# Kernel optimization log

Hardware: AMD Instinct MI355X
Metric: run time of the kernel (lower is better)

Reference implementation:

```python
import jax, jax.numpy as jnp
import numpy as np
from jax import lax

IMG = 512            # image H = W
FH = FW = 32         # feature map spatial size
A = 9                # anchors per location (3 sizes x 3 ratios)
N = FH * FW * A      # total anchors = 9216
IOU_THR = 0.7
MIN_SCORE = 0.5
MIN_SIZE = 1e-3


def make_anchors():
    """Anchors in centroid format (cx, cy, w, h), ordered (H, W, A)."""
    stride = IMG / FH
    sizes = np.array([32.0, 64.0, 128.0])
    ratios = np.array([0.5, 1.0, 2.0])
    ws = (sizes[:, None] / np.sqrt(ratios)[None, :]).reshape(-1)  # (A,)
    hs = (sizes[:, None] * np.sqrt(ratios)[None, :]).reshape(-1)  # (A,)
    cx = (np.arange(FW) + 0.5) * stride
    cy = (np.arange(FH) + 0.5) * stride
    CX = np.broadcast_to(cx[None, :, None], (FH, FW, A))
    CY = np.broadcast_to(cy[:, None, None], (FH, FW, A))
    Wg = np.broadcast_to(ws[None, None, :], (FH, FW, A))
    Hg = np.broadcast_to(hs[None, None, :], (FH, FW, A))
    anc = np.stack([CX, CY, Wg, Hg], axis=-1).reshape(-1, 4)
    return jnp.asarray(anc, dtype=jnp.float32)


def pairwise_iou(b):
    # b: (N,4) corners x1,y1,x2,y2
    x1, y1, x2, y2 = b[:, 0], b[:, 1], b[:, 2], b[:, 3]
    area = (x2 - x1) * (y2 - y1)
    ix1 = jnp.maximum(x1[:, None], x1[None, :])
    iy1 = jnp.maximum(y1[:, None], y1[None, :])
    ix2 = jnp.minimum(x2[:, None], x2[None, :])
    iy2 = jnp.minimum(y2[:, None], y2[None, :])
    inter = jnp.maximum(ix2 - ix1, 0.0) * jnp.maximum(iy2 - iy1, 0.0)
    union = area[:, None] + area[None, :] - inter
    return inter / jnp.maximum(union, 1e-9)


def nms_keep(boxes, scores, valid):
    """Greedy NMS. Returns bool keep mask of shape (N,). Index decisions only."""
    s = jnp.where(valid, scores, -jnp.inf)
    order = jnp.argsort(-s)
    b = boxes[order]
    v = valid[order]
    ious = pairwise_iou(b)  # (N, N)
    idx = jnp.arange(N)

    def body(i, supp):
        keep_i = (~supp[i]) & v[i]
        return supp | (keep_i & (ious[i] > IOU_THR) & (idx > i))

    supp = lax.fori_loop(0, N, body, jnp.zeros(N, dtype=bool))
    keep_sorted = (~supp) & v
    return jnp.zeros(N, dtype=bool).at[order].set(keep_sorted)


def setup_inputs() -> dict:
    key = jax.random.key(0)
    ks = jax.random.split(key, 4)
    return {
        "feature_map": jax.random.normal(ks[0], (1, 256, FH, FW), jnp.float32),
        "conv1_w": jax.random.normal(ks[1], (512, 256, 3, 3), jnp.float32) * 0.02,
        "conv1_b": jnp.zeros((512,), jnp.float32),
        "conv2_w": jax.random.normal(ks[2], (A, 512), jnp.float32) * 0.01,
        "conv2_b": jnp.zeros((A,), jnp.float32),
        "conv3_w": jax.random.normal(ks[3], (4 * A, 512), jnp.float32) * 0.01,
        "conv3_b": jnp.zeros((4 * A,), jnp.float32),
    }


def reference(feature_map, conv1_w, conv1_b, conv2_w, conv2_b, conv3_w, conv3_b):
    anchors = make_anchors()  # (N,4) cx,cy,w,h

    # --- conv backbone head ---
    h = lax.conv_general_dilated(
        feature_map, conv1_w, (1, 1), "SAME",
        dimension_numbers=("NCHW", "OIHW", "NCHW"))
    h = jax.nn.relu(h + conv1_b[None, :, None, None])  # (1,512,H,W)

    scores = jax.nn.sigmoid(
        jnp.einsum("bchw,ac->bahw", h, conv2_w) + conv2_b[None, :, None, None])
    scores = scores.transpose(0, 2, 3, 1).reshape(-1)  # (N,) ordered (H,W,A)

    off = jnp.einsum("bchw,oc->bohw", h, conv3_w) + conv3_b[None, :, None, None]
    off = off.reshape(1, A, 4, FH, FW).transpose(0, 3, 4, 1, 2).reshape(-1, 4)

    acx, acy, aw, ah = anchors[:, 0], anchors[:, 1], anchors[:, 2], anchors[:, 3]
    cx = acx + off[:, 0] * aw
    cy = acy + off[:, 1] * ah
    bw = aw * jnp.exp(off[:, 2])
    bh = ah * jnp.exp(off[:, 3])
    boxes = jnp.stack([cx - bw / 2, cy - bh / 2, cx + bw / 2, cy + bh / 2], axis=1)

    # --- clip to image ---
    lo = jnp.array([0.0, 0.0, 0.0, 0.0], jnp.float32)
    hi = jnp.array([IMG, IMG, IMG, IMG], jnp.float32)
    boxes = jnp.clip(boxes, lo, hi)

    # --- remove small boxes + score threshold (as a mask, jit-safe) ---
    valid = ((boxes[:, 2] - boxes[:, 0]) >= MIN_SIZE) \
          & ((boxes[:, 3] - boxes[:, 1]) >= MIN_SIZE) \
          & (scores >= MIN_SCORE)

    # --- NMS (selection is index-based; no gradient through the decision) ---
    keep = nms_keep(lax.stop_gradient(boxes), lax.stop_gradient(scores), valid)

    out = jnp.concatenate(
        [boxes * keep[:, None].astype(boxes.dtype),
         (scores * keep.astype(scores.dtype))[:, None]], axis=1)  # (N,5)
    return out
```

## Files before the change

### kernel.cpp

```cpp
#include <hip/hip_runtime.h>
#include <math.h>

#define FHW   32
#define NA    9
#define NBOX  9216
#define C1    256
#define C2    512
#define KTOT  2304
#define KS    8
#define KCH   (KTOT / KS)
#define CAP   64
#define ECAP  12288

struct AnchorWH { float w[NA]; float h[NA]; };

#define FP_OFF    0u
#define WT_OFF    1183744u
#define HP_OFF    5902336u
#define BOX_OFF   22679552u
#define SC_OFF    22827008u
#define VL_OFF    22863872u
#define DEG_OFF   22900736u
#define ADJ_OFF   22937600u
#define NV_OFF    24117248u

__global__ __launch_bounds__(256) void k_prep(const float* __restrict__ fin,
                                              float* __restrict__ Fp,
                                              unsigned int* __restrict__ deg,
                                              unsigned int* __restrict__ nv,
                                              const float* __restrict__ w1,
                                              float* __restrict__ Wt) {
    if (blockIdx.x < 1156) {
        int idx = blockIdx.x * 256 + threadIdx.x;
        if (idx < 256 * 34 * 34) {
            int c   = idx / 1156;
            int rem = idx - c * 1156;
            int yy  = rem / 34;
            int xx  = rem - yy * 34;
            float v = 0.f;
            if (yy >= 1 && yy <= 32 && xx >= 1 && xx <= 32)
                v = fin[c * 1024 + (yy - 1) * 32 + (xx - 1)];
            Fp[idx] = v;
        }
        if (idx < NBOX) deg[idx] = 0u;
        if (idx == 0)   *nv = 0u;
    } else {
        __shared__ float tile[32][33];
        int tb  = blockIdx.x - 1156;
        int k0  = (tb % 72) * 32;
        int oc0 = (tb / 72) * 32;
        int t   = threadIdx.x;
        int r0 = t >> 5, c = t & 31;
        #pragma unroll
        for (int i = 0; i < 4; ++i) {
            int r = r0 + 8 * i;
            tile[r][c] = w1[(oc0 + r) * KTOT + k0 + c];
        }
        __syncthreads();
        #pragma unroll
        for (int i = 0; i < 4; ++i) {
            int kk = r0 + 8 * i;
            Wt[(k0 + kk) * C2 + oc0 + c] = tile[c][kk];
        }
    }
}

__global__ __launch_bounds__(256, 2) void k_gemm(const float* __restrict__ Fp,
                                                 const float* __restrict__ Wt,
                                                 float* __restrict__ hp) {
    const int id = blockIdx.x;
    const int bx = id >> 5, g = id & 31;
    const int by = g >> 3, kz = g & 7;
    const int p0  = bx * 64;
    const int oc0 = by * 128;
    const int k0b = kz * KCH;
    const int t  = threadIdx.x;
    const int ty = t >> 4, tx = t & 15;

    __shared__ float As[16][64];
    __shared__ float Bs[16][128];

    float acc[4][8];
    #pragma unroll
    for (int r = 0; r < 4; ++r)
        #pragma unroll
        for (int c = 0; c < 8; ++c) acc[r][c] = 0.f;

    for (int kt = 0; kt < KCH; kt += 16) {
        #pragma unroll
        for (int i = 0; i < 4; ++i) {
            int e  = t + 256 * i;
            int kk = e >> 6, pp = e & 63;
            int k   = k0b + kt + kk;
            int c   = k / 9;
            int kap = k - c * 9;
            int dy  = kap / 3;
            int dx  = kap - dy * 3;
            int p  = p0 + pp;
            int y  = p >> 5, x = p & 31;
            As[kk][pp] = Fp[(c * 34 + y + dy) * 34 + x + dx];
        }
        #pragma unroll
        for (int i = 0; i < 2; ++i) {
            int e4 = t + 256 * i;
            int kk = e4 >> 5, c4 = e4 & 31;
            *(float4*)&Bs[kk][c4 * 4] =
                *(const float4*)&Wt[(k0b + kt + kk) * C2 + oc0 + c4 * 4];
        }
        __syncthreads();
        #pragma unroll
        for (int kk = 0; kk < 16; ++kk) {
            float a[4], b[8];
            *(float4*)&a[0] = *(const float4*)&As[kk][ty * 4];
            *(float4*)&b[0] = *(const float4*)&Bs[kk][tx * 4];
            *(float4*)&b[4] = *(const float4*)&Bs[kk][tx * 4 + 64];
            #pragma unroll
            for (int r = 0; r < 4; ++r)
                #pragma unroll
                for (int c = 0; c < 8; ++c) acc[r][c] += a[r] * b[c];
        }
        __syncthreads();
    }
    #pragma unroll
    for (int r = 0; r < 4; ++r) {
        int p = p0 + ty * 4 + r;
        float* dst = hp + ((kz * 1024 + p) * C2 + oc0 + tx * 4);
        *(float4*)dst        = *(float4*)&acc[r][0];
        *(float4*)(dst + 64) = *(float4*)&acc[r][4];
    }
}

__global__ __launch_bounds__(256) void k_heads(const float* __restrict__ hp,
                                               const float* __restrict__ b1,
                                               const float* __restrict__ w2,
                                               const float* __restrict__ b2,
                                               const float* __restrict__ w3,
                                               const float* __restrict__ b3,
                                               float* __restrict__ boxes,
                                               float* __restrict__ scoresG,
                                               unsigned int* __restrict__ nv,
                                               unsigned int* __restrict__ vlist,
                                               AnchorWH awh) {
    const int p0 = blockIdx.x * 4;
    const int t  = threadIdx.x;
    __shared__ float hrow[4][C2];
    __shared__ float arr[4][45];

    #pragma unroll
    for (int px = 0; px < 4; ++px) {
        int p = p0 + px;
        #pragma unroll
        for (int i = 0; i < 2; ++i) {
            int c = t + 256 * i;
            float s = b1[c];
            #pragma unroll
            for (int ks = 0; ks < KS; ++ks) s += hp[(ks * 1024 + p) * C2 + c];
            hrow[px][c] = fmaxf(s, 0.f);
        }
    }
    __syncthreads();

    const int w = t >> 6, lane = t & 63;
    for (int job = w; job < 180; job += 4) {
        int px = job / 45, j = job - px * 45;
        const float* wp = (j < 9) ? (w2 + j * C2) : (w3 + (j - 9) * C2);
        float s = 0.f;
        #pragma unroll
        for (int i = 0; i < 8; ++i) s += hrow[px][lane + 64 * i] * wp[lane + 64 * i];
        #pragma unroll
        for (int d = 1; d < 64; d <<= 1) s += __shfl_xor(s, d, 64);
        if (lane == 0) arr[px][j] = s;
    }
    __syncthreads();

    if (t < 36) {
        int px = t / 9, a = t - px * 9;
        int p = p0 + px;
        float logit = arr[px][a] + b2[a];
        float score = 1.f / (1.f + expf(-logit));
        float o0 = arr[px][9 + a * 4 + 0] + b3[a * 4 + 0];
        float o1 = arr[px][9 + a * 4 + 1] + b3[a * 4 + 1];
        float o2 = arr[px][9 + a * 4 + 2] + b3[a * 4 + 2];
        float o3 = arr[px][9 + a * 4 + 3] + b3[a * 4 + 3];
        int y = p >> 5, x = p & 31;
        float ax = (x + 0.5f) * 16.f, ay = (y + 0.5f) * 16.f;
        float aw = awh.w[a], ah = awh.h[a];
        float cx = ax + o0 * aw;
        float cy = ay + o1 * ah;
        float bw = aw * expf(o2);
        float bh = ah * expf(o3);
        float x1 = fminf(fmaxf(cx - bw * 0.5f, 0.f), 512.f);
        float y1 = fminf(fmaxf(cy - bh * 0.5f, 0.f), 512.f);
        float x2 = fminf(fmaxf(cx + bw * 0.5f, 0.f), 512.f);
        float y2 = fminf(fmaxf(cy + bh * 0.5f, 0.f), 512.f);
        int n = p * 9 + a;
        float4 bx4; bx4.x = x1; bx4.y = y1; bx4.z = x2; bx4.w = y2;
        ((float4*)boxes)[n] = bx4;
        scoresG[n] = score;
        bool valid = (x2 - x1 >= 0.001f) && (y2 - y1 >= 0.001f) && (score >= 0.5f);
        if (valid) {
            unsigned int ci = atomicAdd(nv, 1u);
            vlist[ci] = (unsigned int)n;
        }
    }
}

__global__ __launch_bounds__(256) void k_adj(const unsigned int* __restrict__ nvp,
                                             const unsigned int* __restrict__ vlist,
                                             const float* __restrict__ boxes,
                                             const float* __restrict__ scoresG,
                                             unsigned int* __restrict__ deg,
                                             unsigned short* __restrict__ adj) {
    const int Nv = (int)*nvp;
    int b = blockIdx.x;
    int tv = (int)(sqrtf(2.f * b + 0.25f) - 0.5f);
    while ((tv + 1) * (tv + 2) / 2 <= b) tv++;
    while (tv * (tv + 1) / 2 > b) tv--;
    int tu = b - tv * (tv + 1) / 2;
    if (tv * 128 >= Nv) return;

    __shared__ float4 ub[128], vb[128];
    __shared__ float  us[128], vs[128];
    __shared__ int    uo[128], vo[128];
    int t = threadIdx.x;
    if (t < 128) {
        int gi = tu * 128 + t;
        if (gi < Nv) { int n = (int)vlist[gi]; ub[t] = ((const float4*)boxes)[n]; us[t] = scoresG[n]; uo[t] = n; }
        else us[t] = -1.f;
    } else {
        int tt = t - 128;
        int gj = tv * 128 + tt;
        if (gj < Nv) { int n = (int)vlist[gj]; vb[tt] = ((const float4*)boxes)[n]; vs[tt] = scoresG[n]; vo[tt] = n; }
        else vs[tt] = -1.f;
    }
    __syncthreads();

    for (int s = 0; s < 64; ++s) {
        int q  = t + 256 * s;
        int i  = q >> 7, jj = q & 127;
        if (tu == tv && i >= jj) continue;
        float su = us[i], sv = vs[jj];
        if (su < 0.f || sv < 0.f) continue;
        float4 bu = ub[i], bv = vb[jj];
        float au = (bu.z - bu.x) * (bu.w - bu.y);
        float av = (bv.z - bv.x) * (bv.w - bv.y);
        float ix1 = fmaxf(bu.x, bv.x), iy1 = fmaxf(bu.y, bv.y);
        float ix2 = fminf(bu.z, bv.z), iy2 = fminf(bu.w, bv.w);
        float inter = fmaxf(ix2 - ix1, 0.f) * fmaxf(iy2 - iy1, 0.f);
        float uni = au + av - inter;
        float iou = inter / fmaxf(uni, 1e-9f);
        if (iou > 0.7f) {
            int gi = tu * 128 + i, gj = tv * 128 + jj;
            bool uHigh = (su > sv) || (su == sv && uo[i] < vo[jj]);
            int lower = uHigh ? gj : gi;
            int upper = uHigh ? gi : gj;
            unsigned int slot = atomicAdd(&deg[lower], 1u);
            if (slot < CAP) adj[lower * CAP + slot] = (unsigned short)upper;
        }
    }
}

__global__ __launch_bounds__(512) void k_peel(const unsigned int* __restrict__ nvp,
                                              const unsigned int* __restrict__ vlist,
                                              const unsigned int* __restrict__ degG,
                                              const unsigned short* __restrict__ adjG,
                                              const float* __restrict__ boxes,
                                              const float* __restrict__ scoresG,
                                              float* __restrict__ out) {
    __shared__ unsigned char  st[NBOX];
    __shared__ unsigned char  degL[NBOX];
    __shared__ unsigned short offL[NBOX];
    __shared__ unsigned short csr[ECAP];
    __shared__ unsigned int   scratch[512];
    __shared__ int changed;
    const int t  = threadIdx.x;
    const int Nv = (int)*nvp;
    const int chunk = (Nv + 511) / 512;
    const int i0 = t * chunk;
    const int i1 = (i0 + chunk < Nv) ? (i0 + chunk) : Nv;

    unsigned int lsum = 0;
    for (int i = i0; i < i1; ++i) {
        unsigned int d = degG[i];
        if (d > CAP) d = CAP;
        degL[i] = (unsigned char)d;
        st[i] = 0;
        lsum += d;
    }
    scratch[t] = lsum;
    __syncthreads();
    for (int ofs = 1; ofs < 512; ofs <<= 1) {
        unsigned int v = (t >= ofs) ? scratch[t - ofs] : 0u;
        __syncthreads();
        scratch[t] += v;
        __syncthreads();
    }
    unsigned int base = scratch[t] - lsum;
    {
        unsigned int off = base;
        for (int i = i0; i < i1; ++i) {
            unsigned int o = (off < ECAP) ? off : ECAP;
            offL[i] = (unsigned short)o;
            int d = degL[i];
            int ld = (int)ECAP - (int)o; if (ld > d) ld = d; if (ld < 0) ld = 0;
            for (int s = 0; s < ld; ++s)
                csr[o + s] = adjG[i * CAP + s];
            off += d;
        }
    }
    __syncthreads();

    for (int round = 0; round < 256; ++round) {
        if (t == 0) changed = 0;
        __syncthreads();
        bool any = false;
        for (int i = i0; i < i1; ++i) {
            if (st[i] == 0) {
                int d   = degL[i];
                int off = offL[i];
                int ld  = (int)ECAP - off; if (ld > d) ld = d; if (ld < 0) ld = 0;
                bool kseen = false, useen = false;
                for (int s = 0; s < d; ++s) {
                    int j = (s < ld) ? (int)csr[off + s] : (int)adjG[i * CAP + s];
                    unsigned char v = st[j];
                    kseen |= (v == 1);
                    useen |= (v == 0);
                }
                if (kseen)       { st[i] = 2; any = true; }
                else if (!useen) { st[i] = 1; any = true; }
            }
        }
        if (any) changed = 1;
        __syncthreads();
        int c = changed;
        __syncthreads();
        if (!c) break;
    }

    for (int n = t; n < NBOX; n += 512) {
        out[n * 5 + 0] = 0.f; out[n * 5 + 1] = 0.f; out[n * 5 + 2] = 0.f;
        out[n * 5 + 3] = 0.f; out[n * 5 + 4] = 0.f;
    }
    __syncthreads();
    for (int i = t; i < Nv; i += 512) {
        if (st[i] == 1) {
            int n = (int)vlist[i];
            float4 b = ((const float4*)boxes)[n];
            out[n * 5 + 0] = b.x;
            out[n * 5 + 1] = b.y;
            out[n * 5 + 2] = b.z;
            out[n * 5 + 3] = b.w;
            out[n * 5 + 4] = scoresG[n];
        }
    }
}

extern "C" void kernel_launch(void* const* d_in, const int* in_sizes, int n_in,
                              void* d_out, int out_size, void* d_ws, size_t ws_size,
                              hipStream_t stream) {
    const float* fin = (const float*)d_in[0];
    const float* w1  = (const float*)d_in[1];
    const float* b1  = (const float*)d_in[2];
    const float* w2  = (const float*)d_in[3];
    const float* b2  = (const float*)d_in[4];
    const float* w3  = (const float*)d_in[5];
    const float* b3  = (const float*)d_in[6];
    float* out = (float*)d_out;

    char* ws = (char*)d_ws;
    float*          Fp    = (float*)(ws + FP_OFF);
    float*          Wt    = (float*)(ws + WT_OFF);
    float*          hp    = (float*)(ws + HP_OFF);
    float*          boxes = (float*)(ws + BOX_OFF);
    float*          sc    = (float*)(ws + SC_OFF);
    unsigned int*   vlist = (unsigned int*)(ws + VL_OFF);
    unsigned int*   deg   = (unsigned int*)(ws + DEG_OFF);
    unsigned short* adj   = (unsigned short*)(ws + ADJ_OFF);
    unsigned int*   nv    = (unsigned int*)(ws + NV_OFF);

    AnchorWH awh;
    {
        const double sizes[3]  = {32.0, 64.0, 128.0};
        const double ratios[3] = {0.5, 1.0, 2.0};
        for (int si = 0; si < 3; ++si)
            for (int ri = 0; ri < 3; ++ri) {
                awh.w[si * 3 + ri] = (float)(sizes[si] / sqrt(ratios[ri]));
                awh.h[si * 3 + ri] = (float)(sizes[si] * sqrt(ratios[ri]));
            }
    }

    k_prep<<<dim3(1156 + 72 * 16), 256, 0, stream>>>(fin, Fp, deg, nv, w1, Wt);
    k_gemm<<<dim3(512), 256, 0, stream>>>(Fp, Wt, hp);
    k_heads<<<dim3(256), 256, 0, stream>>>(hp, b1, w2, b2, w3, b3, boxes, sc, nv, vlist, awh);
    k_adj<<<dim3(72 * 73 / 2), 256, 0, stream>>>(nv, vlist, boxes, sc, deg, adj);
    k_peel<<<dim3(1), 512, 0, stream>>>(nv, vlist, deg, adj, boxes, sc, out);
}
```

Baseline: 229.3 us.

## Move output scatter out of single-block peel and trim peel round overhead

The single-block peel kernel no longer zeroes and writes the whole (N,5) output. It records keep flags in a global buffer, and a new grid-wide k_out kernel writes the masked boxes and scores in parallel. The peel loop now walks only still-undecided nodes through a per-thread bitmask and marks zero-degree nodes as kept up front. It also takes degree from CSR offset differences, enlarges the shared CSR capacity, and uses a per-round flag array so each round needs one barrier instead of three. The cost is one extra kernel launch, plus a round cap lowered from 256 to 96, which could end peeling early on very deep suppression chains.

```diff
diff --git a/kernel.cpp b/kernel.cpp
--- a/kernel.cpp
+++ b/kernel.cpp
@@ -10,7 +10,8 @@
 #define KS    8
 #define KCH   (KTOT / KS)
 #define CAP   64
-#define ECAP  12288
+#define ECAP  16384
+#define ROUNDS 96
 
 struct AnchorWH { float w[NA]; float h[NA]; };
 
@@ -22,11 +23,13 @@
 #define VL_OFF    22863872u
 #define DEG_OFF   22900736u
 #define ADJ_OFF   22937600u
-#define NV_OFF    24117248u
+#define KEEP_OFF  24117248u
+#define NV_OFF    24154112u
 
 __global__ __launch_bounds__(256) void k_prep(const float* __restrict__ fin,
                                               float* __restrict__ Fp,
                                               unsigned int* __restrict__ deg,
+                                              unsigned int* __restrict__ keepG,
                                               unsigned int* __restrict__ nv,
                                               const float* __restrict__ w1,
                                               float* __restrict__ Wt) {
@@ -42,7 +45,7 @@
                 v = fin[c * 1024 + (yy - 1) * 32 + (xx - 1)];
             Fp[idx] = v;
         }
-        if (idx < NBOX) deg[idx] = 0u;
+        if (idx < NBOX) { deg[idx] = 0u; keepG[idx] = 0u; }
         if (idx == 0)   *nv = 0u;
     } else {
         __shared__ float tile[32][33];
@@ -264,27 +267,25 @@
                                               const unsigned int* __restrict__ vlist,
                                               const unsigned int* __restrict__ degG,
                                               const unsigned short* __restrict__ adjG,
-                                              const float* __restrict__ boxes,
-                                              const float* __restrict__ scoresG,
-                                              float* __restrict__ out) {
+                                              unsigned int* __restrict__ keepG) {
+    __shared__ unsigned short offL[NBOX + 2];
     __shared__ unsigned char  st[NBOX];
-    __shared__ unsigned char  degL[NBOX];
-    __shared__ unsigned short offL[NBOX];
     __shared__ unsigned short csr[ECAP];
     __shared__ unsigned int   scratch[512];
-    __shared__ int changed;
+    __shared__ unsigned char  flags[ROUNDS];
     const int t  = threadIdx.x;
     const int Nv = (int)*nvp;
     const int chunk = (Nv + 511) / 512;
     const int i0 = t * chunk;
     const int i1 = (i0 + chunk < Nv) ? (i0 + chunk) : Nv;
 
+    if (t < ROUNDS) flags[t] = 0;
+
     unsigned int lsum = 0;
     for (int i = i0; i < i1; ++i) {
         unsigned int d = degG[i];
         if (d > CAP) d = CAP;
-        degL[i] = (unsigned char)d;
-        st[i] = 0;
+        st[i] = (unsigned char)d;
         lsum += d;
     }
     scratch[t] = lsum;
@@ -295,64 +296,72 @@
         scratch[t] += v;
         __syncthreads();
     }
-    unsigned int base = scratch[t] - lsum;
+    if (t == 511) {
+        unsigned int tot = scratch[511];
+        offL[Nv] = (unsigned short)(tot < ECAP ? tot : ECAP);
+    }
+    unsigned int amask = 0;
     {
-        unsigned int off = base;
+        unsigned int off = scratch[t] - lsum;
         for (int i = i0; i < i1; ++i) {
             unsigned int o = (off < ECAP) ? off : ECAP;
             offL[i] = (unsigned short)o;
-            int d = degL[i];
+            int d = st[i];
             int ld = (int)ECAP - (int)o; if (ld > d) ld = d; if (ld < 0) ld = 0;
             for (int s = 0; s < ld; ++s)
                 csr[o + s] = adjG[i * CAP + s];
             off += d;
+            if (d == 0) st[i] = 1;
+            else { st[i] = 0; amask |= 1u << (i - i0); }
         }
     }
     __syncthreads();
 
-    for (int round = 0; round < 256; ++round) {
-        if (t == 0) changed = 0;
-        __syncthreads();
+    for (int r = 0; r < ROUNDS; ++r) {
         bool any = false;
-        for (int i = i0; i < i1; ++i) {
-            if (st[i] == 0) {
-                int d   = degL[i];
-                int off = offL[i];
-                int ld  = (int)ECAP - off; if (ld > d) ld = d; if (ld < 0) ld = 0;
-                bool kseen = false, useen = false;
-                for (int s = 0; s < d; ++s) {
-                    int j = (s < ld) ? (int)csr[off + s] : (int)adjG[i * CAP + s];
-                    unsigned char v = st[j];
-                    kseen |= (v == 1);
-                    useen |= (v == 0);
-                }
-                if (kseen)       { st[i] = 2; any = true; }
-                else if (!useen) { st[i] = 1; any = true; }
+        unsigned int m = amask;
+        while (m) {
+            int b = __ffs(m) - 1; m &= m - 1;
+            int i = i0 + b;
+            int o = offL[i], on = offL[i + 1];
+            int d, ld;
+            if (on < ECAP) { d = on - o; ld = d; }
+            else {
+                unsigned int dg = degG[i]; d = (dg > CAP) ? CAP : (int)dg;
+                ld = (int)ECAP - o; if (ld < 0) ld = 0; if (ld > d) ld = d;
             }
-        }
-        if (any) changed = 1;
-        __syncthreads();
-        int c = changed;
-        __syncthreads();
-        if (!c) break;
-    }
-
-    for (int n = t; n < NBOX; n += 512) {
-        out[n * 5 + 0] = 0.f; out[n * 5 + 1] = 0.f; out[n * 5 + 2] = 0.f;
-        out[n * 5 + 3] = 0.f; out[n * 5 + 4] = 0.f;
-    }
-    __syncthreads();
-    for (int i = t; i < Nv; i += 512) {
-        if (st[i] == 1) {
-            int n = (int)vlist[i];
-            float4 b = ((const float4*)boxes)[n];
-            out[n * 5 + 0] = b.x;
-            out[n * 5 + 1] = b.y;
-            out[n * 5 + 2] = b.z;
-            out[n * 5 + 3] = b.w;
-            out[n * 5 + 4] = scoresG[n];
-        }
-    }
+            bool kseen = false, useen = false;
+            for (int s = 0; s < d; ++s) {
+                int j = (s < ld) ? (int)csr[o + s] : (int)adjG[i * CAP + s];
+                unsigned char v = st[j];
+                kseen |= (v == 1);
+                useen |= (v == 0);
+            }
+            if (kseen)       { st[i] = 2; any = true; amask &= ~(1u << b); }
+            else if (!useen) { st[i] = 1; any = true; amask &= ~(1u << b); }
+        }
+        if (any) flags[r] = 1;
+        __syncthreads();
+        if (!flags[r]) break;
+    }
+
+    for (int i = i0; i < i1; ++i)
+        if (st[i] == 1) keepG[vlist[i]] = 1u;
+}
+
+__global__ __launch_bounds__(256) void k_out(const float* __restrict__ boxes,
+                                             const float* __restrict__ scoresG,
+                                             const unsigned int* __restrict__ keepG,
+                                             float* __restrict__ out) {
+    int n = blockIdx.x * 256 + threadIdx.x;
+    if (n >= NBOX) return;
+    float k = keepG[n] ? 1.f : 0.f;
+    float4 b = ((const float4*)boxes)[n];
+    out[n * 5 + 0] = b.x * k;
+    out[n * 5 + 1] = b.y * k;
+    out[n * 5 + 2] = b.z * k;
+    out[n * 5 + 3] = b.w * k;
+    out[n * 5 + 4] = scoresG[n] * k;
 }
 
 extern "C" void kernel_launch(void* const* d_in, const int* in_sizes, int n_in,
@@ -376,6 +385,7 @@
     unsigned int*   vlist = (unsigned int*)(ws + VL_OFF);
     unsigned int*   deg   = (unsigned int*)(ws + DEG_OFF);
     unsigned short* adj   = (unsigned short*)(ws + ADJ_OFF);
+    unsigned int*   keepG = (unsigned int*)(ws + KEEP_OFF);
     unsigned int*   nv    = (unsigned int*)(ws + NV_OFF);
 
     AnchorWH awh;
@@ -389,9 +399,10 @@
             }
     }
 
-    k_prep<<<dim3(1156 + 72 * 16), 256, 0, stream>>>(fin, Fp, deg, nv, w1, Wt);
+    k_prep<<<dim3(1156 + 72 * 16), 256, 0, stream>>>(fin, Fp, deg, keepG, nv, w1, Wt);
     k_gemm<<<dim3(512), 256, 0, stream>>>(Fp, Wt, hp);
     k_heads<<<dim3(256), 256, 0, stream>>>(hp, b1, w2, b2, w3, b3, boxes, sc, nv, vlist, awh);
     k_adj<<<dim3(72 * 73 / 2), 256, 0, stream>>>(nv, vlist, boxes, sc, deg, adj);
-    k_peel<<<dim3(1), 512, 0, stream>>>(nv, vlist, deg, adj, boxes, sc, out);
-}
+    k_peel<<<dim3(1), 512, 0, stream>>>(nv, vlist, deg, adj, keepG);
+    k_out<<<dim3((NBOX + 255) / 256), 256, 0, stream>>>(boxes, sc, keepG, out);
+}
```

Measured after the change: 203.7 us. -11.2%, faster.
